# Performance work log

Measured on AMD Instinct MI355X. Metric: run time of the kernel, lower is better.

The kernel has to match this reference:

```python
import jax, jax.numpy as jnp
import numpy as np

NR, NS = 4, 3      # num_rotations, num_scales
RP, SP = 2, 2      # rotation_size, scale_size
K = 5              # kernel_size
PAD = 2
STRIDE = 1
NF = 9             # num basis functions (effective_size**2)


def setup_inputs() -> dict:
    key = jax.random.key(0)
    k1, k2, k3 = jax.random.split(key, 3)
    x = jax.random.normal(k1, (8, 16, NR * NS, 128, 128), dtype=jnp.float32)
    weight = jax.random.normal(k2, (16, 16, RP * SP, NF), dtype=jnp.float32) * 0.05
    basis = jax.random.normal(k3, (NF, NR * NS, K, K), dtype=jnp.float32)
    return {"x": x, "weight": weight, "basis": basis}


def reference(x, weight, basis):
    B, C, S, H, W = x.shape
    out_c, in_c, _, nf = weight.shape
    nrs = NR * NS
    # kernel synthesis: weight @ basis -> [nrs, out, in, RP*SP, K, K]
    kernel = jnp.einsum('oirf,fgxy->goirxy', weight, basis)
    kernel = kernel.reshape(nrs * out_c, in_c, RP, SP, K, K)
    # reshape input to [B, C, NR, NS, H, W]
    xg = x.reshape(B, C, NR, NS, H, W)
    # zero-pad scale axis at the end by SP-1
    xg = jnp.pad(xg, ((0, 0), (0, 0), (0, 0), (0, SP - 1), (0, 0), (0, 0)))
    # circular-pad rotation axis at the end by RP-1 (wrap from beginning)
    xg = jnp.concatenate([xg, xg[:, :, :RP - 1]], axis=2)
    out = None
    for i in range(RP):
        for j in range(SP):
            xs = xg[:, :, i:i + NR, j:j + NS]                     # [B,C,NR,NS,H,W]
            xs = xs.transpose(0, 2, 3, 1, 4, 5).reshape(B, nrs * C, H, W)
            o = jax.lax.conv_general_dilated(
                xs, kernel[:, :, i, j],
                window_strides=(STRIDE, STRIDE),
                padding=[(PAD, PAD), (PAD, PAD)],
                feature_group_count=nrs,
                dimension_numbers=('NCHW', 'OIHW', 'NCHW'))
            out = o if out is None else out + o
    B_, C_, H_, W_ = out.shape
    out = out.reshape(B_, nrs, out_c, H_, W_).transpose(0, 2, 1, 3, 4)
    return out
```

## Files before the change

### kernel.cpp

```cpp
#include <hip/hip_runtime.h>


#define NRS 12
#define CIN 16
#define COUT 16
#define HW 128
#define IMG (HW*HW)
#define ICSTRIDE (NRS*IMG)

#define HALO_H 36
#define HALO_W 20
#define ROWB2 640
#define NCHUNK 1440
#define BUFB 24576
#define PADW 132
#define PADROWB (PADW*32)

#define S_NPIX (HALO_H*HALO_W)
#define S_HALFB (S_NPIX*16)
#define S_ROWB (HALO_W*16)

typedef __bf16 bf16x8 __attribute__((ext_vector_type(8)));
typedef float  f32x4  __attribute__((ext_vector_type(4)));

__device__ __forceinline__ unsigned short f2bf(float f) {
    unsigned u = __builtin_bit_cast(unsigned, f);
    u += 0x7fffu + ((u >> 16) & 1u);
    return (unsigned short)(u >> 16);
}

__global__ void build_kc(const float* __restrict__ wgt, const float* __restrict__ basis,
                         unsigned short* __restrict__ kc) {
    int idx = blockIdx.x * 256 + threadIdx.x;
    const int total = 12 * 4 * 13 * 16 * 32;
    if (idx >= total) return;
    int k  = idx & 31;
    int possel = k >> 4, ic = k & 15;
    int o  = (idx >> 5) & 15;
    int t2 = idx >> 9;
    int pp = t2 % 13;
    int gr = t2 / 13;
    int rbase = gr & 3, g = gr >> 2;
    int pos = 2 * pp + possel;
    float s = 0.f;
    if (pos < 25) {
        int xk = pos / 5, yk = pos - 5 * xk;
        #pragma unroll
        for (int f = 0; f < 9; ++f)
            s = fmaf(wgt[((o * CIN + ic) * 4 + rbase) * 9 + f],
                     basis[((f * NRS + g) * 5 + xk) * 5 + yk], s);
    }
    kc[idx] = f2bf(s);
}

__global__ void cvt_pad(const float* __restrict__ x, unsigned short* __restrict__ xbf) {
    int idx = blockIdx.x * 256 + threadIdx.x;
    const int total = 8 * 12 * PADW * PADW;
    if (idx >= total) return;
    int wp = idx % PADW;
    int t1 = idx / PADW;
    int hp = t1 % PADW;
    int bs = t1 / PADW;
    int s  = bs % 12, bb = bs / 12;
    int h = hp - 2, w = wp - 2;
    bool ok = ((unsigned)h < 128u) && ((unsigned)w < 128u);
    const float* px = x + ((size_t)bb * 192 + s) * IMG + h * HW + w;
    unsigned short v[16];
    #pragma unroll
    for (int ic = 0; ic < 16; ++ic) {
        float f = 0.f;
        if (ok) f = px[(size_t)ic * ICSTRIDE];
        v[ic] = f2bf(f);
    }
    uint4 lo, hi;
    lo.x = v[0] | (v[1] << 16);  lo.y = v[2] | (v[3] << 16);
    lo.z = v[4] | (v[5] << 16);  lo.w = v[6] | (v[7] << 16);
    hi.x = v[8] | (v[9] << 16);  hi.y = v[10] | (v[11] << 16);
    hi.z = v[12] | (v[13] << 16); hi.w = v[14] | (v[15] << 16);
    *(uint4*)(xbf + (size_t)idx * 16)     = lo;
    *(uint4*)(xbf + (size_t)idx * 16 + 8) = hi;
}

__global__ __launch_bounds__(256, 2)
void conv_fast(const unsigned short* __restrict__ xbf, const unsigned short* __restrict__ kc,
               float* __restrict__ out) {
    const int b   = blockIdx.z;
    const int r0  = blockIdx.y;
    const int th0 = (blockIdx.x >> 3) * 32;
    const int tw0 = (blockIdx.x & 7) * 16;

    const int t    = threadIdx.x;
    const int lane = t & 63;
    const int wave = t >> 6;
    const int n    = lane & 15;
    const int q    = lane >> 4;
    const int possel = q >> 1;
    const int half_  = q & 1;

    __shared__ uint4 xs4[(2 * BUFB) / 16];
    char* xsc = (char*)xs4;

    int soff[6];
    #pragma unroll
    for (int j = 0; j < 6; ++j) {
        int c = wave * 384 + j * 64 + lane;
        if (c < NCHUNK) {
            int rl = c / 40, rem = c - rl * 40;
            int hf = rem / 20, cl = rem - hf * 20;
            soff[j] = rl * PADROWB + cl * 32 + hf * 16;
        } else soff[j] = 0;
    }

    int boff[13];
    #pragma unroll
    for (int pp = 0; pp < 13; ++pp) {
        int pos = 2 * pp + possel; if (pos > 24) pos = 24;
        int dx = pos / 5, dy = pos - 5 * dx;
        boff[pp] = dx * ROWB2 + half_ * 320 + (n + dy) * 16;
    }
    const int aoff = n * 32 + q * 8;

    f32x4 acc[3][8];
    #pragma unroll
    for (int s0 = 0; s0 < 3; ++s0)
        #pragma unroll
        for (int pg = 0; pg < 8; ++pg) acc[s0][pg] = (f32x4){0.f, 0.f, 0.f, 0.f};

    const char* xb0 = (const char*)xbf;
    const size_t tileoff = ((size_t)th0 * PADW + tw0) * 32;

    {
        const char* sb = xb0 + ((size_t)(b * 12 + r0 * 3) * PADW * PADW) * 32 + tileoff;
        char* lb = xsc + wave * 6144;
        #pragma unroll
        for (int j = 0; j < 6; ++j)
            __builtin_amdgcn_global_load_lds(
                (const __attribute__((address_space(1))) void*)(sb + soff[j]),
                (__attribute__((address_space(3))) void*)(lb + j * 1024), 16, 0, 0);
    }
    __syncthreads();
    int cur = 0;

    #pragma unroll 1
    for (int i = 0; i < 2; ++i) {
        int rr = r0 + i; if (rr >= 4) rr -= 4;
        int rrn = rr + 1; if (rrn >= 4) rrn -= 4;
        #pragma unroll
        for (int ss = 0; ss < 3; ++ss) {
            if (i == 0 || ss < 2) {
                int sin_next = (ss < 2) ? (rr * 3 + ss + 1) : (rrn * 3);
                const char* sb = xb0 + ((size_t)(b * 12 + sin_next) * PADW * PADW) * 32 + tileoff;
                char* lb = xsc + (cur ^ 1) * BUFB + wave * 6144;
                #pragma unroll
                for (int j = 0; j < 6; ++j)
                    __builtin_amdgcn_global_load_lds(
                        (const __attribute__((address_space(1))) void*)(sb + soff[j]),
                        (__attribute__((address_space(3))) void*)(lb + j * 1024), 16, 0, 0);
            }

            const unsigned short* kc0 = kc + (size_t)((r0 * 3 + ss) * 4 + 2 * i) * (13 * 512);
            const char* wb = xsc + cur * BUFB + wave * 8 * ROWB2;
            if (ss > 0) {
                const unsigned short* kc1 = kc + (size_t)((r0 * 3 + ss - 1) * 4 + 2 * i + 1) * (13 * 512);
                #pragma unroll
                for (int pp = 0; pp < 13; ++pp) {
                    bf16x8 af0 = *(const bf16x8*)(kc0 + pp * 512 + aoff);
                    bf16x8 af1 = *(const bf16x8*)(kc1 + pp * 512 + aoff);
                    const char* wp = wb + boff[pp];
                    #pragma unroll
                    for (int pg = 0; pg < 8; ++pg) {
                        bf16x8 bfv = *(const bf16x8*)(wp + pg * ROWB2);
                        acc[ss][pg]     = __builtin_amdgcn_mfma_f32_16x16x32_bf16(af0, bfv, acc[ss][pg], 0, 0, 0);
                        acc[ss - 1][pg] = __builtin_amdgcn_mfma_f32_16x16x32_bf16(af1, bfv, acc[ss - 1][pg], 0, 0, 0);
                    }
                }
            } else {
                #pragma unroll
                for (int pp = 0; pp < 13; ++pp) {
                    bf16x8 af0 = *(const bf16x8*)(kc0 + pp * 512 + aoff);
                    const char* wp = wb + boff[pp];
                    #pragma unroll
                    for (int pg = 0; pg < 8; ++pg) {
                        bf16x8 bfv = *(const bf16x8*)(wp + pg * ROWB2);
                        acc[ss][pg] = __builtin_amdgcn_mfma_f32_16x16x32_bf16(af0, bfv, acc[ss][pg], 0, 0, 0);
                    }
                }
            }
            __syncthreads();
            cur ^= 1;
        }
    }

    #pragma unroll
    for (int s0 = 0; s0 < 3; ++s0) {
        const size_t obase = ((size_t)b * COUT * NRS + (r0 * 3 + s0)) * IMG;
        #pragma unroll
        for (int pg = 0; pg < 8; ++pg) {
            int row = th0 + wave * 8 + pg;
            int col = tw0 + n;
            size_t pix = (size_t)row * HW + col;
            #pragma unroll
            for (int r = 0; r < 4; ++r) {
                int o = q * 4 + r;
                out[obase + (size_t)o * NRS * IMG + pix] = acc[s0][pg][r];
            }
        }
    }
}

__global__ __launch_bounds__(256, 2)
void conv_slow(const float* __restrict__ x, const unsigned short* __restrict__ kc,
               float* __restrict__ out) {
    const int b   = blockIdx.z;
    const int r0  = blockIdx.y;
    const int th0 = (blockIdx.x >> 3) * 32;
    const int tw0 = (blockIdx.x & 7) * 16;

    const int t    = threadIdx.x;
    const int lane = t & 63;
    const int wave = t >> 6;
    const int n    = lane & 15;
    const int q    = lane >> 4;
    const int possel = q >> 1;
    const int half_  = q & 1;

    __shared__ uint4 xs4[(2 * S_HALFB) / 16];
    char* xsc = (char*)xs4;

    int boff[13];
    #pragma unroll
    for (int pp = 0; pp < 13; ++pp) {
        int pos = 2 * pp + possel; if (pos > 24) pos = 24;
        int dx = pos / 5, dy = pos - 5 * dx;
        boff[pp] = half_ * S_HALFB + dx * S_ROWB + (n + dy) * 16;
    }
    const int aoff = n * 32 + q * 8;

    f32x4 acc[3][8];
    #pragma unroll
    for (int s0 = 0; s0 < 3; ++s0)
        #pragma unroll
        for (int pg = 0; pg < 8; ++pg) acc[s0][pg] = (f32x4){0.f, 0.f, 0.f, 0.f};

    #pragma unroll 1
    for (int i = 0; i < 2; ++i) {
        int rr = r0 + i; if (rr >= 4) rr -= 4;
        #pragma unroll
        for (int ss = 0; ss < 3; ++ss) {
            const int sin_ = rr * 3 + ss;
            const float* xb = x + ((size_t)b * CIN * NRS + sin_) * IMG;

            __syncthreads();
            for (int p = t; p < S_NPIX; p += 256) {
                int rl = p / HALO_W, cl = p - rl * HALO_W;
                int hh = th0 + rl - 2, ww = tw0 + cl - 2;
                bool ok = ((unsigned)hh < 128u) && ((unsigned)ww < 128u);
                const float* px = xb + hh * HW + ww;
                unsigned short v[16];
                #pragma unroll
                for (int ic = 0; ic < 16; ++ic) {
                    float f = 0.f;
                    if (ok) f = px[(size_t)ic * ICSTRIDE];
                    v[ic] = f2bf(f);
                }
                uint4 lo, hi;
                lo.x = v[0] | (v[1] << 16);  lo.y = v[2] | (v[3] << 16);
                lo.z = v[4] | (v[5] << 16);  lo.w = v[6] | (v[7] << 16);
                hi.x = v[8] | (v[9] << 16);  hi.y = v[10] | (v[11] << 16);
                hi.z = v[12] | (v[13] << 16); hi.w = v[14] | (v[15] << 16);
                *(uint4*)(xsc + p * 16)           = lo;
                *(uint4*)(xsc + S_HALFB + p * 16) = hi;
            }
            __syncthreads();

            const unsigned short* kc0 = kc + (size_t)((r0 * 3 + ss) * 4 + 2 * i) * (13 * 512);
            const unsigned short* kc1 = kc + (size_t)((r0 * 3 + ss - 1) * 4 + 2 * i + 1) * (13 * 512);
            const char* wb = xsc + wave * 8 * S_ROWB;
            #pragma unroll
            for (int pp = 0; pp < 13; ++pp) {
                bf16x8 af0 = *(const bf16x8*)(kc0 + pp * 512 + aoff);
                bf16x8 af1;
                if (ss > 0) af1 = *(const bf16x8*)(kc1 + pp * 512 + aoff);
                const char* wp = wb + boff[pp];
                #pragma unroll
                for (int pg = 0; pg < 8; ++pg) {
                    bf16x8 bfv = *(const bf16x8*)(wp + pg * S_ROWB);
                    acc[ss][pg] = __builtin_amdgcn_mfma_f32_16x16x32_bf16(af0, bfv, acc[ss][pg], 0, 0, 0);
                    if (ss > 0)
                        acc[ss - 1][pg] = __builtin_amdgcn_mfma_f32_16x16x32_bf16(af1, bfv, acc[ss - 1][pg], 0, 0, 0);
                }
            }
        }
    }

    #pragma unroll
    for (int s0 = 0; s0 < 3; ++s0) {
        const size_t obase = ((size_t)b * COUT * NRS + (r0 * 3 + s0)) * IMG;
        #pragma unroll
        for (int pg = 0; pg < 8; ++pg) {
            int row = th0 + wave * 8 + pg;
            int col = tw0 + n;
            size_t pix = (size_t)row * HW + col;
            #pragma unroll
            for (int r = 0; r < 4; ++r) {
                int o = q * 4 + r;
                out[obase + (size_t)o * NRS * IMG + pix] = acc[s0][pg][r];
            }
        }
    }
}

extern "C" void kernel_launch(void* const* d_in, const int* in_sizes, int n_in,
                              void* d_out, int out_size, void* d_ws, size_t ws_size,
                              hipStream_t stream) {
    const float* x      = (const float*)d_in[0];
    const float* weight = (const float*)d_in[1];
    const float* basis  = (const float*)d_in[2];
    float* out = (float*)d_out;
    unsigned short* kc = (unsigned short*)d_ws;

    build_kc<<<dim3((12 * 4 * 13 * 16 * 32 + 255) / 256), dim3(256), 0, stream>>>(weight, basis, kc);

    const size_t xbf_off = 655360;
    const size_t xbf_bytes = (size_t)8 * 12 * PADW * PADW * 32;
    if (ws_size >= xbf_off + xbf_bytes) {
        unsigned short* xbf = (unsigned short*)((char*)d_ws + xbf_off);
        cvt_pad<<<dim3((8 * 12 * PADW * PADW + 255) / 256), dim3(256), 0, stream>>>(x, xbf);
        conv_fast<<<dim3(32, 4, 8), dim3(256), 0, stream>>>(xbf, kc, out);
    } else {
        conv_slow<<<dim3(32, 4, 8), dim3(256), 0, stream>>>(x, kc, out);
    }
}
```

Measured before the change: 253.7 us.

## Stage halo tiles through registers instead of direct global-to-LDS loads

Replaces the asynchronous global_load_lds copies with ordinary vector loads into registers. They are issued before the MFMA loop, and the registers are written to the alternate LDS buffer after the compute. The chunk-to-thread mapping is now linear across the block, which packs the LDS buffer tightly and shrinks each buffer from 24576 to 23040 bytes. This aims to cut wasted LDS space and possibly improve occupancy. In exchange it adds 24 VGPRs of staging per thread plus explicit LDS store instructions.

```diff
diff --git a/kernel.cpp b/kernel.cpp
--- a/kernel.cpp
+++ b/kernel.cpp
@@ -12,7 +12,7 @@
 #define HALO_W 20
 #define ROWB2 640
 #define NCHUNK 1440
-#define BUFB 24576
+#define BUFB 23040
 #define PADW 132
 #define PADROWB (PADW*32)
 
@@ -100,15 +100,14 @@
     __shared__ uint4 xs4[(2 * BUFB) / 16];
     char* xsc = (char*)xs4;
 
+    const bool tail_ok = (t < NCHUNK - 5 * 256);
     int soff[6];
     #pragma unroll
     for (int j = 0; j < 6; ++j) {
-        int c = wave * 384 + j * 64 + lane;
-        if (c < NCHUNK) {
-            int rl = c / 40, rem = c - rl * 40;
-            int hf = rem / 20, cl = rem - hf * 20;
-            soff[j] = rl * PADROWB + cl * 32 + hf * 16;
-        } else soff[j] = 0;
+        int c = t + j * 256; if (c >= NCHUNK) c = NCHUNK - 1;
+        int rl = c / 40, rem = c - rl * 40;
+        int hf = rem / 20, cl = rem - hf * 20;
+        soff[j] = rl * PADROWB + cl * 32 + hf * 16;
     }
 
     int boff[13];
@@ -129,14 +128,14 @@
     const char* xb0 = (const char*)xbf;
     const size_t tileoff = ((size_t)th0 * PADW + tw0) * 32;
 
+    uint4 st[6];
     {
         const char* sb = xb0 + ((size_t)(b * 12 + r0 * 3) * PADW * PADW) * 32 + tileoff;
-        char* lb = xsc + wave * 6144;
-        #pragma unroll
-        for (int j = 0; j < 6; ++j)
-            __builtin_amdgcn_global_load_lds(
-                (const __attribute__((address_space(1))) void*)(sb + soff[j]),
-                (__attribute__((address_space(3))) void*)(lb + j * 1024), 16, 0, 0);
+        #pragma unroll
+        for (int j = 0; j < 6; ++j) st[j] = *(const uint4*)(sb + soff[j]);
+        #pragma unroll
+        for (int j = 0; j < 5; ++j) *(uint4*)(xsc + (t + j * 256) * 16) = st[j];
+        if (tail_ok) *(uint4*)(xsc + (t + 1280) * 16) = st[5];
     }
     __syncthreads();
     int cur = 0;
@@ -147,15 +146,12 @@
         int rrn = rr + 1; if (rrn >= 4) rrn -= 4;
         #pragma unroll
         for (int ss = 0; ss < 3; ++ss) {
-            if (i == 0 || ss < 2) {
+            const bool has_next = (i == 0 || ss < 2);
+            if (has_next) {
                 int sin_next = (ss < 2) ? (rr * 3 + ss + 1) : (rrn * 3);
                 const char* sb = xb0 + ((size_t)(b * 12 + sin_next) * PADW * PADW) * 32 + tileoff;
-                char* lb = xsc + (cur ^ 1) * BUFB + wave * 6144;
-                #pragma unroll
-                for (int j = 0; j < 6; ++j)
-                    __builtin_amdgcn_global_load_lds(
-                        (const __attribute__((address_space(1))) void*)(sb + soff[j]),
-                        (__attribute__((address_space(3))) void*)(lb + j * 1024), 16, 0, 0);
+                #pragma unroll
+                for (int j = 0; j < 6; ++j) st[j] = *(const uint4*)(sb + soff[j]);
             }
 
             const unsigned short* kc0 = kc + (size_t)((r0 * 3 + ss) * 4 + 2 * i) * (13 * 512);
@@ -186,6 +182,13 @@
                     }
                 }
             }
+
+            if (has_next) {
+                char* lb = xsc + (cur ^ 1) * BUFB;
+                #pragma unroll
+                for (int j = 0; j < 5; ++j) *(uint4*)(lb + (t + j * 256) * 16) = st[j];
+                if (tail_ok) *(uint4*)(lb + (t + 1280) * 16) = st[5];
+            }
             __syncthreads();
             cur ^= 1;
         }
```

Result: slower. 287.2 us (+13.2%).
